# Kernel optimization log

Hardware: AMD Instinct MI355X
Metric: run time of the kernel (lower is better)

The kernel has to match this reference:

```python
import jax, jax.numpy as jnp
import numpy as np

N = 2000      # num_of_vertices
T = 12        # history
B = 4         # batch
C = 32        # in_dim == out_dims[i]
STRIDES = 3
L = 3         # len(out_dims)
W_WIN = T - STRIDES + 1  # 10 sliding windows


def setup_inputs() -> dict:
    key = jax.random.key(0)
    ks = jax.random.split(key, 12)
    adj_scale = 2.0 / (3 * N)  # keep row sums ~1 so activations stay in range
    fc_scale = 1.0 / np.sqrt(C)
    g_scale = 1.0 / np.sqrt(2 * C)
    return {
        "x": jax.random.normal(ks[0], (B, T, N, C), jnp.float32),
        "adj": jax.random.uniform(ks[1], (3 * N, 3 * N), jnp.float32) * adj_scale,
        "temporal_adj": jax.random.uniform(ks[2], (N, N), jnp.float32) * adj_scale,
        "temporal_embedding": jax.random.normal(ks[3], (1, T, 1, C), jnp.float32) * 0.0003,
        "spatial_embedding": jax.random.normal(ks[4], (1, 1, N, C), jnp.float32) * 0.0003,
        "W_fc": jax.random.normal(ks[5], (W_WIN, L, C, 2 * C), jnp.float32) * fc_scale,
        "b_fc": jnp.zeros((W_WIN, L, 2 * C), jnp.float32),
        "Wr": jax.random.normal(ks[6], (2 * C, C), jnp.float32) * g_scale,
        "br": jnp.zeros((C,), jnp.float32),
        "Wu": jax.random.normal(ks[7], (2 * C, C), jnp.float32) * g_scale,
        "bu": jnp.zeros((C,), jnp.float32),
        "Wn": jax.random.normal(ks[8], (2 * C, C), jnp.float32) * g_scale,
        "bn": jnp.zeros((C,), jnp.float32),
        "Wo": jax.random.normal(ks[9], (C, C), jnp.float32) * (1.0 / np.sqrt(C)),
        "bo": jnp.zeros((C,), jnp.float32),
    }


def _forward(x, adj, temporal_adj, temporal_embedding, spatial_embedding,
             W_fc, b_fc, Wr, br, Wu, bu, Wn, bn, Wo, bo):
    # x: (B, T, N, C)
    x = x + temporal_embedding + spatial_embedding

    # Patch the 3Nx3N adjacency: 4 corner N x N blocks become temporal_adj
    A = adj.at[:N, :N].set(temporal_adj)
    A = A.at[2 * N:, 2 * N:].set(temporal_adj)
    A = A.at[2 * N:, :N].set(temporal_adj)
    A = A.at[:N, 2 * N:].set(temporal_adj)

    # Extract all sliding windows at once: (B, W, 3, N, C)
    idx = jnp.arange(W_WIN)[:, None] + jnp.arange(STRIDES)[None, :]
    xw = x[:, idx]
    # -> (W, 3N, B, C) matching torch reshape(B, 3*N, C).permute(1,0,2)
    h = jnp.transpose(xw, (1, 2, 3, 0, 4)).reshape(W_WIN, STRIDES * N, B, C)

    # STSGCM stack (per-window weights), GLU activation
    layer_mid = []
    for l in range(L):
        h = jnp.einsum('nm,wmbc->wnbc', A, h)                 # graph conv
        z = jnp.einsum('wnbc,wcd->wnbd', h, W_fc[:, l]) + b_fc[:, l][:, None, None, :]
        lhs, rhs = jnp.split(z, 2, axis=-1)
        h = lhs * jax.nn.sigmoid(rhs)                         # GLU
        layer_mid.append(h[:, N:2 * N])                       # middle time slice (W, N, B, C)
    out = jnp.max(jnp.stack(layer_mid, axis=0), axis=0)      # max over layers
    out = jnp.transpose(out, (2, 0, 1, 3))                    # (B, W, N, C)

    # GRU-style gating across the W time slices (note: next hidden is yt)
    def step(hid, inp):
        comb = jnp.concatenate([inp, hid], axis=-1)
        reset = jax.nn.sigmoid(comb @ Wr + br)
        update = jax.nn.sigmoid(comb @ Wu + bu)
        comb_new = jnp.concatenate([inp, reset * hid], axis=-1)
        new_mem = jnp.tanh(comb_new @ Wn + bn)
        output = update * hid + (1.0 - update) * new_mem
        yt = jax.nn.sigmoid(output @ Wo + bo)
        return yt, output

    h0 = jnp.zeros((B, N, C), x.dtype)
    _, residual = jax.lax.scan(step, h0, jnp.transpose(out, (1, 0, 2, 3)))
    residual = jnp.transpose(residual, (1, 0, 2, 3))          # (B, W, N, C)
    return out + residual


def reference(x, adj, temporal_adj, temporal_embedding, spatial_embedding,
              W_fc, b_fc, Wr, br, Wu, bu, Wn, bn, Wo, bo):
    return _forward(x, adj, temporal_adj, temporal_embedding, spatial_embedding,
                    W_fc, b_fc, Wr, br, Wu, bu, Wn, bn, Wo, bo)
```

## Files before the change

kernel.cpp:

```cpp
#include <hip/hip_runtime.h>
#include <hip/hip_bf16.h>

#define N_NODE 2000
#define BB 4
#define CC 32
#define LL 3
#define WW 10
#define M3 6000
#define MP 6016
#define KP 6016
#define NCOL 1280

typedef __bf16 bf16x8 __attribute__((ext_vector_type(8)));
typedef float f32x4 __attribute__((ext_vector_type(4)));
typedef unsigned short ushort8 __attribute__((ext_vector_type(8)));

__device__ __forceinline__ float sigmoidf_(float x) { return 1.0f / (1.0f + __expf(-x)); }
__device__ __forceinline__ float tanhf_(float x) { return 1.0f - 2.0f / (__expf(2.0f * x) + 1.0f); }

__global__ __launch_bounds__(256) void k_build_A(const float* __restrict__ adj,
                                                 const float* __restrict__ tadj,
                                                 __hip_bfloat16* __restrict__ A) {
  const int m8 = blockIdx.x * 256 + threadIdx.x;
  const int m = m8 * 8;
  const int n = blockIdx.y;
  if (m >= KP) return;
  ushort8 out = {0, 0, 0, 0, 0, 0, 0, 0};
  if (n < M3 && m < M3) {
    const bool nr = (n < N_NODE) | (n >= 2 * N_NODE);
    const bool mr = (m < N_NODE) | (m >= 2 * N_NODE);
    const float* src;
    if (nr & mr) {
      const int nn = (n >= 2 * N_NODE) ? n - 2 * N_NODE : n;
      const int mm = (m >= 2 * N_NODE) ? m - 2 * N_NODE : m;
      src = tadj + (size_t)nn * N_NODE + mm;
    } else {
      src = adj + (size_t)n * M3 + m;
    }
#pragma unroll
    for (int j = 0; j < 8; ++j) {
      union { __hip_bfloat16 h; unsigned short u; } cv;
      cv.h = __float2bfloat16(src[j]);
      out[j] = cv.u;
    }
  }
  *(ushort8*)(A + (size_t)n * KP + m) = out;
}

__global__ __launch_bounds__(256) void k_build_H(const float* __restrict__ x,
                                                 const float* __restrict__ temb,
                                                 const float* __restrict__ semb,
                                                 __hip_bfloat16* __restrict__ H) {
  const int m = blockIdx.x * 256 + threadIdx.x;
  const int col = blockIdx.y;
  if (m >= KP) return;
  float v = 0.0f;
  if (m < M3) {
    const int w = col >> 7, b = (col >> 5) & 3, c = col & 31;
    const int s = (m >= 2 * N_NODE) ? 2 : (m >= N_NODE ? 1 : 0);
    const int n = m - s * N_NODE;
    const int tt = w + s;
    v = x[(((size_t)b * 12 + tt) * N_NODE + n) * CC + c] + temb[tt * CC + c] +
        semb[(size_t)n * CC + c];
  }
  H[(size_t)col * KP + m] = __float2bfloat16(v);
}

__global__ __launch_bounds__(256) void k_gemm(const __hip_bfloat16* __restrict__ A,
                                              const __hip_bfloat16* __restrict__ Bt,
                                              float* __restrict__ G) {
  __shared__ __align__(16) char lA[128 * 128];
  __shared__ __align__(16) char lB[128 * 128];
  const int tid = threadIdx.x;
  const int lane = tid & 63;
  const int wv = tid >> 6;
  const int wr = wv >> 1, wc = wv & 1;

  const int bid = blockIdx.x + 47 * (blockIdx.y + 10 * blockIdx.z);
  const int q = 940 / 8, r = 940 % 8;
  const int xcd = bid & 7, lid = bid >> 3;
  const int swz = (xcd < r ? xcd * (q + 1) : r * (q + 1) + (xcd - r) * q) + lid;
  const int bx = swz % 47;
  const int tmp = swz / 47;
  const int by = tmp % 10;
  const int kt0 = (tmp / 10) * 47;
  const long row0 = (long)bx * 128;
  const long col0 = (long)by * 128;

  const int srow = wv * 32 + (lane >> 3);
  const int soff = ((lane & 7) ^ (lane >> 3)) << 4;
  const char* gA = (const char*)A + (size_t)(row0 + srow) * (KP * 2) + soff;
  const char* gB = (const char*)Bt + (size_t)(col0 + srow) * (KP * 2) + soff;
  const size_t rstep = (size_t)8 * KP * 2;

  const int rrow = lane & 15;
  const int off0 = (((lane >> 4) << 4)) ^ ((lane & 7) << 4);
  const int off1 = (64 | ((lane >> 4) << 4)) ^ ((lane & 7) << 4);

  f32x4 acc[4][4] = {};

  for (int kt = kt0; kt < kt0 + 47; ++kt) {
    __syncthreads();
    const char* ga = gA + (size_t)kt * 128;
    const char* gb = gB + (size_t)kt * 128;
#pragma unroll
    for (int i = 0; i < 4; ++i) {
      __builtin_amdgcn_global_load_lds(
          (const __attribute__((address_space(1))) void*)(ga + (size_t)i * rstep),
          (__attribute__((address_space(3))) void*)(lA + wv * 4096 + i * 1024), 16, 0, 0);
    }
#pragma unroll
    for (int i = 0; i < 4; ++i) {
      __builtin_amdgcn_global_load_lds(
          (const __attribute__((address_space(1))) void*)(gb + (size_t)i * rstep),
          (__attribute__((address_space(3))) void*)(lB + wv * 4096 + i * 1024), 16, 0, 0);
    }
    __syncthreads();
#pragma unroll
    for (int ks = 0; ks < 2; ++ks) {
      const int offk = ks ? off1 : off0;
      bf16x8 af[4], bfr[4];
#pragma unroll
      for (int mi = 0; mi < 4; ++mi)
        af[mi] = *(const bf16x8*)(lA + (wr * 64 + mi * 16 + rrow) * 128 + offk);
#pragma unroll
      for (int ni = 0; ni < 4; ++ni)
        bfr[ni] = *(const bf16x8*)(lB + (wc * 64 + ni * 16 + rrow) * 128 + offk);
#pragma unroll
      for (int mi = 0; mi < 4; ++mi)
#pragma unroll
        for (int ni = 0; ni < 4; ++ni)
          acc[mi][ni] =
              __builtin_amdgcn_mfma_f32_16x16x32_bf16(af[mi], bfr[ni], acc[mi][ni], 0, 0, 0);
    }
  }
  const int crow = (lane >> 4) * 4;
  const int ccol = lane & 15;
#pragma unroll
  for (int mi = 0; mi < 4; ++mi) {
#pragma unroll
    for (int ni = 0; ni < 4; ++ni) {
      const long r_ = row0 + wr * 64 + mi * 16 + crow;
      const long cix = col0 + wc * 64 + ni * 16 + ccol;
      float* gp = G + (size_t)r_ * NCOL + cix;
#pragma unroll
      for (int j = 0; j < 4; ++j) atomicAdd(gp + (size_t)j * NCOL, acc[mi][ni][j]);
    }
  }
}

__global__ __launch_bounds__(256) void k_fcglu(const float* __restrict__ G,
                                               const float* __restrict__ Wfc,
                                               const float* __restrict__ bfc,
                                               __hip_bfloat16* __restrict__ Hn,
                                               float* __restrict__ outb, int l, int writeH) {
  __shared__ float sW[32 * 64];
  __shared__ float sb[64];
  const int w = blockIdx.y;
  const int t = threadIdx.x;
  const float* Ws = Wfc + (size_t)(w * LL + l) * 32 * 64;
#pragma unroll
  for (int i = 0; i < 8; ++i) sW[t + 256 * i] = Ws[t + 256 * i];
  if (t < 64) sb[t] = bfc[(size_t)(w * LL + l) * 64 + t];
  __syncthreads();
  const int nl = t >> 2, b = t & 3;
  const int n = blockIdx.x * 64 + nl;
  const int colbase = w * 128 + b * 32;
  if (n >= M3) {
    if (writeH) {
      for (int c = 0; c < 32; ++c) Hn[(size_t)(colbase + c) * KP + n] = __float2bfloat16(0.0f);
    }
    return;
  }
  const float* g = G + (size_t)n * NCOL + colbase;
  float z[64];
#pragma unroll
  for (int d = 0; d < 64; ++d) z[d] = sb[d];
  for (int c = 0; c < 32; ++c) {
    const float gv = g[c];
#pragma unroll
    for (int d = 0; d < 64; ++d) z[d] = fmaf(gv, sW[c * 64 + d], z[d]);
  }
  float h[32];
#pragma unroll
  for (int c = 0; c < 32; ++c) h[c] = z[c] * sigmoidf_(z[32 + c]);
  if (writeH) {
#pragma unroll
    for (int c = 0; c < 32; ++c) Hn[(size_t)(colbase + c) * KP + n] = __float2bfloat16(h[c]);
  }
  if (n >= N_NODE && n < 2 * N_NODE) {
    float* op = outb + (((size_t)b * WW + w) * N_NODE + (n - N_NODE)) * CC;
    if (l == 0) {
#pragma unroll
      for (int c = 0; c < 32; ++c) op[c] = h[c];
    } else {
#pragma unroll
      for (int c = 0; c < 32; ++c) op[c] = fmaxf(op[c], h[c]);
    }
  }
}

__global__ __launch_bounds__(256) void k_gru_all(float* __restrict__ outb,
                                                 const float* __restrict__ Wr,
                                                 const float* __restrict__ brr,
                                                 const float* __restrict__ Wu,
                                                 const float* __restrict__ bu,
                                                 const float* __restrict__ Wn,
                                                 const float* __restrict__ bnn,
                                                 const float* __restrict__ Wo,
                                                 const float* __restrict__ bo) {
  __shared__ float sWr[2048], sWu[2048], sWn[2048], sWo[1024];
  __shared__ float sbr[32], sbu[32], sbn[32], sbo[32];
  __shared__ float sI[8][32], sH[8][32], sT[8][32];
  const int t = threadIdx.x;
  for (int i = t; i < 2048; i += 256) {
    sWr[i] = Wr[i];
    sWu[i] = Wu[i];
    sWn[i] = Wn[i];
  }
  for (int i = t; i < 1024; i += 256) sWo[i] = Wo[i];
  if (t < 32) {
    sbr[t] = brr[t];
    sbu[t] = bu[t];
    sbn[t] = bnn[t];
    sbo[t] = bo[t];
  }
  __syncthreads();
  const int g = t >> 5, c = t & 31;
  const int n = blockIdx.x * 8 + g;
  const int b = blockIdx.y;
  float hid = 0.0f;
  for (int w = 0; w < WW; ++w) {
    const size_t oix = (((size_t)b * WW + w) * N_NODE + n) * CC + c;
    const float inp = outb[oix];
    sI[g][c] = inp;
    sH[g][c] = hid;
    __syncthreads();
    float ar = sbr[c], au = sbu[c];
#pragma unroll 4
    for (int d = 0; d < 32; ++d) {
      const float i_ = sI[g][d], h_ = sH[g][d];
      ar = fmaf(i_, sWr[d * 32 + c], ar);
      ar = fmaf(h_, sWr[(32 + d) * 32 + c], ar);
      au = fmaf(i_, sWu[d * 32 + c], au);
      au = fmaf(h_, sWu[(32 + d) * 32 + c], au);
    }
    const float r = sigmoidf_(ar), u = sigmoidf_(au);
    __syncthreads();
    sT[g][c] = r * hid;
    __syncthreads();
    float an = sbn[c];
#pragma unroll 4
    for (int d = 0; d < 32; ++d) {
      an = fmaf(sI[g][d], sWn[d * 32 + c], an);
      an = fmaf(sT[g][d], sWn[(32 + d) * 32 + c], an);
    }
    const float nm = tanhf_(an);
    const float outv = u * hid + (1.0f - u) * nm;
    __syncthreads();
    sT[g][c] = outv;
    __syncthreads();
    float ay = sbo[c];
#pragma unroll 4
    for (int d = 0; d < 32; ++d) ay = fmaf(sT[g][d], sWo[d * 32 + c], ay);
    hid = sigmoidf_(ay);
    outb[oix] = inp + outv;
    __syncthreads();
  }
}

extern "C" void kernel_launch(void* const* d_in, const int* in_sizes, int n_in, void* d_out,
                              int out_size, void* d_ws, size_t ws_size, hipStream_t stream) {
  const float* x = (const float*)d_in[0];
  const float* adj = (const float*)d_in[1];
  const float* tadj = (const float*)d_in[2];
  const float* temb = (const float*)d_in[3];
  const float* semb = (const float*)d_in[4];
  const float* Wfc = (const float*)d_in[5];
  const float* bfc = (const float*)d_in[6];
  const float* Wr = (const float*)d_in[7];
  const float* brr = (const float*)d_in[8];
  const float* Wu = (const float*)d_in[9];
  const float* bu = (const float*)d_in[10];
  const float* Wn = (const float*)d_in[11];
  const float* bnn = (const float*)d_in[12];
  const float* Wo = (const float*)d_in[13];
  const float* bo = (const float*)d_in[14];
  float* outb = (float*)d_out;

  char* ws = (char*)d_ws;
  const size_t szA = (size_t)MP * KP * 2;
  const size_t szH = (size_t)NCOL * KP * 2;
  const size_t szG = (size_t)MP * NCOL * 4;
  if (ws_size < szA + 2 * szH + szG) return;

  __hip_bfloat16* A = (__hip_bfloat16*)ws;
  __hip_bfloat16* H0 = (__hip_bfloat16*)(ws + szA);
  __hip_bfloat16* H1 = (__hip_bfloat16*)(ws + szA + szH);
  float* G = (float*)(ws + szA + 2 * szH);

  k_build_A<<<dim3(3, KP), 256, 0, stream>>>(adj, tadj, A);
  k_build_H<<<dim3(24, NCOL), 256, 0, stream>>>(x, temb, semb, H0);

  __hip_bfloat16* Hc = H0;
  __hip_bfloat16* Hx = H1;
  for (int l = 0; l < LL; ++l) {
    hipMemsetAsync(G, 0, szG, stream);
    k_gemm<<<dim3(47, 10, 2), 256, 0, stream>>>(A, Hc, G);
    k_fcglu<<<dim3(94, 10), 256, 0, stream>>>(G, Wfc, bfc, Hx, outb, l, l < 2 ? 1 : 0);
    __hip_bfloat16* tmp = Hc;
    Hc = Hx;
    Hx = tmp;
  }
  k_gru_all<<<dim3(250, BB), 256, 0, stream>>>(outb, Wr, brr, Wu, bu, Wn, bnn, Wo, bo);
}
```

Measured before the change: 945.7 us.

## Fuse FC-GLU epilogue into adjacency GEMM and drop split-K atomics

The GEMM now runs the full K range in one block (no split-K), stages the fp32 accumulator tile in LDS, and applies the per-window FC+GLU, H write-back and layer max directly in the epilogue. This removes the G buffer, its memset, the fp32 atomic adds and a separate kernel launch per layer. In exchange the grid halves to 470 blocks with twice the K loop per block, which lowers parallelism on a 256-CU device, and the epilogue adds extra LDS traffic and register pressure.

```diff
diff --git a/kernel.cpp b/kernel.cpp
--- a/kernel.cpp
+++ b/kernel.cpp
@@ -9,7 +9,6 @@
 #define M3 6000
 #define MP 6016
 #define KP 6016
-#define NCOL 1280
 
 typedef __bf16 bf16x8 __attribute__((ext_vector_type(8)));
 typedef float f32x4 __attribute__((ext_vector_type(4)));
@@ -68,24 +67,33 @@
 
 __global__ __launch_bounds__(256) void k_gemm(const __hip_bfloat16* __restrict__ A,
                                               const __hip_bfloat16* __restrict__ Bt,
-                                              float* __restrict__ G) {
-  __shared__ __align__(16) char lA[128 * 128];
-  __shared__ __align__(16) char lB[128 * 128];
+                                              __hip_bfloat16* __restrict__ Hn,
+                                              float* __restrict__ outb,
+                                              const float* __restrict__ Wfc,
+                                              const float* __restrict__ bfc,
+                                              int l, int writeH) {
+  __shared__ __align__(16) char smem[33280];
+  __shared__ float sW[2048];
+  __shared__ float sb[64];
+  char* lA = smem;
+  char* lB = smem + 16384;
   const int tid = threadIdx.x;
   const int lane = tid & 63;
   const int wv = tid >> 6;
   const int wr = wv >> 1, wc = wv & 1;
 
-  const int bid = blockIdx.x + 47 * (blockIdx.y + 10 * blockIdx.z);
-  const int q = 940 / 8, r = 940 % 8;
+  const int bid = blockIdx.x + 47 * blockIdx.y;
+  const int q = 470 / 8, r = 470 % 8;
   const int xcd = bid & 7, lid = bid >> 3;
   const int swz = (xcd < r ? xcd * (q + 1) : r * (q + 1) + (xcd - r) * q) + lid;
   const int bx = swz % 47;
-  const int tmp = swz / 47;
-  const int by = tmp % 10;
-  const int kt0 = (tmp / 10) * 47;
+  const int by = swz / 47;
   const long row0 = (long)bx * 128;
   const long col0 = (long)by * 128;
+
+  const float* Ws = Wfc + ((size_t)by * LL + l) * 2048;
+  for (int i = tid; i < 2048; i += 256) sW[i] = Ws[i];
+  if (tid < 64) sb[tid] = bfc[((size_t)by * LL + l) * 64 + tid];
 
   const int srow = wv * 32 + (lane >> 3);
   const int soff = ((lane & 7) ^ (lane >> 3)) << 4;
@@ -99,7 +107,8 @@
 
   f32x4 acc[4][4] = {};
 
-  for (int kt = kt0; kt < kt0 + 47; ++kt) {
+  const int NKT = KP / 64;
+  for (int kt = 0; kt < NKT; ++kt) {
     __syncthreads();
     const char* ga = gA + (size_t)kt * 128;
     const char* gb = gB + (size_t)kt * 128;
@@ -134,69 +143,60 @@
               __builtin_amdgcn_mfma_f32_16x16x32_bf16(af[mi], bfr[ni], acc[mi][ni], 0, 0, 0);
     }
   }
+
+  __syncthreads();
+  float* gh = (float*)smem;
   const int crow = (lane >> 4) * 4;
   const int ccol = lane & 15;
-#pragma unroll
-  for (int mi = 0; mi < 4; ++mi) {
-#pragma unroll
-    for (int ni = 0; ni < 4; ++ni) {
-      const long r_ = row0 + wr * 64 + mi * 16 + crow;
-      const long cix = col0 + wc * 64 + ni * 16 + ccol;
-      float* gp = G + (size_t)r_ * NCOL + cix;
-#pragma unroll
-      for (int j = 0; j < 4; ++j) atomicAdd(gp + (size_t)j * NCOL, acc[mi][ni][j]);
-    }
-  }
-}
-
-__global__ __launch_bounds__(256) void k_fcglu(const float* __restrict__ G,
-                                               const float* __restrict__ Wfc,
-                                               const float* __restrict__ bfc,
-                                               __hip_bfloat16* __restrict__ Hn,
-                                               float* __restrict__ outb, int l, int writeH) {
-  __shared__ float sW[32 * 64];
-  __shared__ float sb[64];
-  const int w = blockIdx.y;
-  const int t = threadIdx.x;
-  const float* Ws = Wfc + (size_t)(w * LL + l) * 32 * 64;
-#pragma unroll
-  for (int i = 0; i < 8; ++i) sW[t + 256 * i] = Ws[t + 256 * i];
-  if (t < 64) sb[t] = bfc[(size_t)(w * LL + l) * 64 + t];
-  __syncthreads();
-  const int nl = t >> 2, b = t & 3;
-  const int n = blockIdx.x * 64 + nl;
-  const int colbase = w * 128 + b * 32;
-  if (n >= M3) {
+  const int em = tid & 127;
+  const int ebg = tid >> 7;
+  const long row = row0 + em;
+  const bool vrow = row < M3;
+
+#pragma unroll
+  for (int half = 0; half < 2; ++half) {
+    if (wc == half) {
+#pragma unroll
+      for (int mi = 0; mi < 4; ++mi) {
+#pragma unroll
+        for (int ni = 0; ni < 4; ++ni) {
+          const int rbase = wr * 64 + mi * 16 + crow;
+          const int clocal = ni * 16 + ccol;
+#pragma unroll
+          for (int j = 0; j < 4; ++j) gh[(rbase + j) * 65 + clocal] = acc[mi][ni][j];
+        }
+      }
+    }
+    __syncthreads();
+    const int b = half * 2 + ebg;
+    float z[64];
+#pragma unroll
+    for (int d = 0; d < 64; ++d) z[d] = sb[d];
+    for (int c = 0; c < 32; ++c) {
+      const float gv = gh[em * 65 + ebg * 32 + c];
+#pragma unroll
+      for (int d = 0; d < 64; ++d) z[d] = fmaf(gv, sW[c * 64 + d], z[d]);
+    }
+    float h[32];
+#pragma unroll
+    for (int cc = 0; cc < 32; ++cc)
+      h[cc] = vrow ? z[cc] * sigmoidf_(z[32 + cc]) : 0.0f;
     if (writeH) {
-      for (int c = 0; c < 32; ++c) Hn[(size_t)(colbase + c) * KP + n] = __float2bfloat16(0.0f);
-    }
-    return;
-  }
-  const float* g = G + (size_t)n * NCOL + colbase;
-  float z[64];
-#pragma unroll
-  for (int d = 0; d < 64; ++d) z[d] = sb[d];
-  for (int c = 0; c < 32; ++c) {
-    const float gv = g[c];
-#pragma unroll
-    for (int d = 0; d < 64; ++d) z[d] = fmaf(gv, sW[c * 64 + d], z[d]);
-  }
-  float h[32];
-#pragma unroll
-  for (int c = 0; c < 32; ++c) h[c] = z[c] * sigmoidf_(z[32 + c]);
-  if (writeH) {
-#pragma unroll
-    for (int c = 0; c < 32; ++c) Hn[(size_t)(colbase + c) * KP + n] = __float2bfloat16(h[c]);
-  }
-  if (n >= N_NODE && n < 2 * N_NODE) {
-    float* op = outb + (((size_t)b * WW + w) * N_NODE + (n - N_NODE)) * CC;
-    if (l == 0) {
-#pragma unroll
-      for (int c = 0; c < 32; ++c) op[c] = h[c];
-    } else {
-#pragma unroll
-      for (int c = 0; c < 32; ++c) op[c] = fmaxf(op[c], h[c]);
-    }
+#pragma unroll
+      for (int cc = 0; cc < 32; ++cc)
+        Hn[(size_t)(col0 + b * 32 + cc) * KP + row] = __float2bfloat16(h[cc]);
+    }
+    if (row >= N_NODE && row < 2 * N_NODE) {
+      float* op = outb + (((size_t)b * WW + by) * N_NODE + (row - N_NODE)) * CC;
+      if (l == 0) {
+#pragma unroll
+        for (int cc = 0; cc < 32; ++cc) op[cc] = h[cc];
+      } else {
+#pragma unroll
+        for (int cc = 0; cc < 32; ++cc) op[cc] = fmaxf(op[cc], h[cc]);
+      }
+    }
+    __syncthreads();
   }
 }
 
@@ -290,24 +290,20 @@
 
   char* ws = (char*)d_ws;
   const size_t szA = (size_t)MP * KP * 2;
-  const size_t szH = (size_t)NCOL * KP * 2;
-  const size_t szG = (size_t)MP * NCOL * 4;
-  if (ws_size < szA + 2 * szH + szG) return;
+  const size_t szH = (size_t)(WW * 128) * KP * 2;
+  if (ws_size < szA + 2 * szH) return;
 
   __hip_bfloat16* A = (__hip_bfloat16*)ws;
   __hip_bfloat16* H0 = (__hip_bfloat16*)(ws + szA);
   __hip_bfloat16* H1 = (__hip_bfloat16*)(ws + szA + szH);
-  float* G = (float*)(ws + szA + 2 * szH);
 
   k_build_A<<<dim3(3, KP), 256, 0, stream>>>(adj, tadj, A);
-  k_build_H<<<dim3(24, NCOL), 256, 0, stream>>>(x, temb, semb, H0);
+  k_build_H<<<dim3(24, WW * 128), 256, 0, stream>>>(x, temb, semb, H0);
 
   __hip_bfloat16* Hc = H0;
   __hip_bfloat16* Hx = H1;
   for (int l = 0; l < LL; ++l) {
-    hipMemsetAsync(G, 0, szG, stream);
-    k_gemm<<<dim3(47, 10, 2), 256, 0, stream>>>(A, Hc, G);
-    k_fcglu<<<dim3(94, 10), 256, 0, stream>>>(G, Wfc, bfc, Hx, outb, l, l < 2 ? 1 : 0);
+    k_gemm<<<dim3(47, 10), 256, 0, stream>>>(A, Hc, Hx, outb, Wfc, bfc, l, l < 2 ? 1 : 0);
     __hip_bfloat16* tmp = Hc;
     Hc = Hx;
     Hx = tmp;
```

After: 1.180 ms. 24.8% more time.
